# Kernel tuning notes

Measured on AMD Instinct MI355X. Metric: run time of the kernel, lower is better.

## Reference

```python
import jax, jax.numpy as jnp
import numpy as np


def setup_inputs() -> dict:
    key = jax.random.key(0)
    k1, k2 = jax.random.split(key)
    set1 = jax.random.normal(k1, (8192, 256), dtype=jnp.float32)
    set2 = jax.random.normal(k2, (8192, 256), dtype=jnp.float32)
    return {"set1": set1, "set2": set2}


def reference(set1, set2):
    # Pairwise Euclidean distances via the Gram trick:
    sq1 = jnp.sum(set1 * set1, axis=-1)  # [N]
    sq2 = jnp.sum(set2 * set2, axis=-1)  # [M]
    gram = jnp.einsum('nd,md->nm', set1, set2)  # [N,M]
    d2 = sq1[:, None] + sq2[None, :] - 2.0 * gram
    d = jnp.sqrt(jnp.maximum(d2, 0.0))  # clamp tiny negatives from roundoff
    term_1 = jnp.mean(jnp.min(d, axis=1))  # for each point in set1, nearest in set2
    term_2 = jnp.mean(jnp.min(d, axis=0))  # for each point in set2, nearest in set1
    return term_1 + term_2
```

## Files before the change

kernel.cpp:

```cpp
#include <hip/hip_runtime.h>

#define N_PTS 8192
#define D_DIM 256
#define BN 256
#define BM 128
#define BK 64
#define INF_BITS 0x7F800000u

typedef __attribute__((ext_vector_type(8))) short short8;
typedef __attribute__((ext_vector_type(4))) float f32x4;

__device__ __forceinline__ void gload_lds16(const ushort* g, ushort* l) {
    __builtin_amdgcn_global_load_lds(
        (const __attribute__((address_space(1))) void*)g,
        (__attribute__((address_space(3))) void*)l, 16, 0, 0);
}

__device__ __forceinline__ ushort f2bf(float x) {
    unsigned u = __float_as_uint(x);
    return (ushort)((u + 0x7FFFu + ((u >> 16) & 1u)) >> 16);
}

__global__ void prep_kernel(const float* __restrict__ s1, const float* __restrict__ s2,
                            ushort* __restrict__ b1, ushort* __restrict__ b2,
                            float* __restrict__ sq1, float* __restrict__ sq2,
                            unsigned* __restrict__ rowmin2, unsigned* __restrict__ colmin2) {
    const int half = N_PTS * D_DIM;
    int t = blockIdx.x * 256 + threadIdx.x;
    int e = t * 8;
    bool first = e < half;
    const float* src = first ? s1 : s2;
    ushort* dst = first ? b1 : b2;
    int off = first ? e : e - half;
    float4 v0 = *(const float4*)(src + off);
    float4 v1 = *(const float4*)(src + off + 4);
    float s = v0.x * v0.x + v0.y * v0.y + v0.z * v0.z + v0.w * v0.w
            + v1.x * v1.x + v1.y * v1.y + v1.z * v1.z + v1.w * v1.w;
    ushort4 o0 = { f2bf(v0.x), f2bf(v0.y), f2bf(v0.z), f2bf(v0.w) };
    ushort4 o1 = { f2bf(v1.x), f2bf(v1.y), f2bf(v1.z), f2bf(v1.w) };
    *(ushort4*)(dst + off)     = o0;
    *(ushort4*)(dst + off + 4) = o1;
    #pragma unroll
    for (int m = 1; m <= 16; m <<= 1) s += __shfl_xor(s, m, 64);
    int sub = threadIdx.x & 31;
    int row = off >> 8;
    if (sub == 0) (first ? sq1 : sq2)[row] = s;
    if (sub == 1) (first ? rowmin2 : colmin2)[row] = INF_BITS;
}

__global__ __launch_bounds__(256, 2) void tile_kernel(
    const ushort* __restrict__ B1, const ushort* __restrict__ B2,
    const float* __restrict__ sq1, const float* __restrict__ sq2,
    unsigned* __restrict__ rowmin2, unsigned* __restrict__ colmin2) {
    __shared__ ushort As[BN * BK] __attribute__((aligned(16)));
    __shared__ ushort Bs[BM * BK] __attribute__((aligned(16)));
    __shared__ unsigned rs[BN];
    __shared__ unsigned cs[BM];

    const int tid  = threadIdx.x;
    const int lane = tid & 63;
    const int w    = tid >> 6;
    const int quad = lane >> 4;
    const int c    = lane & 15;
    const int n_off = (w >> 1) * 128;
    const int m_off = (w & 1) * 64;
    const int n0 = blockIdx.y * BN;
    const int m0 = blockIdx.x * BM;

    rs[tid] = INF_BITS;
    if (tid < BM) cs[tid] = INF_BITS;

    f32x4 acc[8][4];
    #pragma unroll
    for (int ti = 0; ti < 8; ti++)
        #pragma unroll
        for (int tj = 0; tj < 4; tj++) acc[ti][tj] = (f32x4){0.f, 0.f, 0.f, 0.f};

    for (int k0 = 0; k0 < D_DIM; k0 += BK) {
        #pragma unroll
        for (int r = 0; r < 8; r++) {
            int idx = r * 256 + tid;
            int row = idx >> 3;
            int gc  = (idx & 7) ^ (row & 7);
            gload_lds16(B1 + (size_t)(n0 + row) * D_DIM + k0 + gc * 8,
                        &As[(idx & ~63) * 8]);
        }
        #pragma unroll
        for (int r = 0; r < 4; r++) {
            int idx = r * 256 + tid;
            int row = idx >> 3;
            int gc  = (idx & 7) ^ (row & 7);
            gload_lds16(B2 + (size_t)(m0 + row) * D_DIM + k0 + gc * 8,
                        &Bs[(idx & ~63) * 8]);
        }
        __syncthreads();

        #pragma unroll
        for (int kk = 0; kk < 2; kk++) {
            short8 a[8], b[4];
            #pragma unroll
            for (int ti = 0; ti < 8; ti++) {
                int row = n_off + ti * 16 + c;
                int ch  = (kk * 4 + quad) ^ (row & 7);
                a[ti] = *(const short8*)&As[row * BK + ch * 8];
            }
            #pragma unroll
            for (int tj = 0; tj < 4; tj++) {
                int row = m_off + tj * 16 + c;
                int ch  = (kk * 4 + quad) ^ (row & 7);
                b[tj] = *(const short8*)&Bs[row * BK + ch * 8];
            }
            #pragma unroll
            for (int ti = 0; ti < 8; ti++)
                #pragma unroll
                for (int tj = 0; tj < 4; tj++)
                    acc[ti][tj] = __builtin_amdgcn_mfma_f32_16x16x32_bf16(
                        a[ti], b[tj], acc[ti][tj], 0, 0, 0);
        }
        __syncthreads();
    }

    float sqm[4];
    #pragma unroll
    for (int tj = 0; tj < 4; tj++) sqm[tj] = sq2[m0 + m_off + tj * 16 + c];
    float cmin[4];
    #pragma unroll
    for (int tj = 0; tj < 4; tj++) cmin[tj] = __uint_as_float(INF_BITS);

    #pragma unroll
    for (int ti = 0; ti < 8; ti++) {
        float4 sqn = *(const float4*)&sq1[n0 + n_off + ti * 16 + quad * 4];
        float rmin[4] = { __uint_as_float(INF_BITS), __uint_as_float(INF_BITS),
                          __uint_as_float(INF_BITS), __uint_as_float(INF_BITS) };
        #pragma unroll
        for (int tj = 0; tj < 4; tj++) {
            float sn[4] = { sqn.x, sqn.y, sqn.z, sqn.w };
            #pragma unroll
            for (int r = 0; r < 4; r++) {
                float d2 = fmaxf(sn[r] + sqm[tj] - 2.f * acc[ti][tj][r], 0.f);
                rmin[r]  = fminf(rmin[r], d2);
                cmin[tj] = fminf(cmin[tj], d2);
            }
        }
        #pragma unroll
        for (int m = 1; m <= 8; m <<= 1)
            #pragma unroll
            for (int r = 0; r < 4; r++)
                rmin[r] = fminf(rmin[r], __shfl_xor(rmin[r], m, 64));
        if (c == 0) {
            #pragma unroll
            for (int r = 0; r < 4; r++)
                atomicMin(&rs[n_off + ti * 16 + quad * 4 + r], __float_as_uint(rmin[r]));
        }
    }
    #pragma unroll
    for (int m = 16; m <= 32; m <<= 1)
        #pragma unroll
        for (int tj = 0; tj < 4; tj++)
            cmin[tj] = fminf(cmin[tj], __shfl_xor(cmin[tj], m, 64));
    if (quad == 0) {
        #pragma unroll
        for (int tj = 0; tj < 4; tj++)
            atomicMin(&cs[m_off + tj * 16 + c], __float_as_uint(cmin[tj]));
    }
    __syncthreads();

    atomicMin(&rowmin2[n0 + tid], rs[tid]);
    if (tid < BM) atomicMin(&colmin2[m0 + tid], cs[tid]);
}

__global__ __launch_bounds__(1024) void reduce_kernel(const unsigned* __restrict__ mins,
                                                      float* __restrict__ out) {
    int tid = threadIdx.x;
    uint4 v[4];
    #pragma unroll
    for (int j = 0; j < 4; j++) v[j] = ((const uint4*)mins)[j * 1024 + tid];
    float s = 0.f;
    #pragma unroll
    for (int j = 0; j < 4; j++)
        s += sqrtf(__uint_as_float(v[j].x)) + sqrtf(__uint_as_float(v[j].y))
           + sqrtf(__uint_as_float(v[j].z)) + sqrtf(__uint_as_float(v[j].w));
    #pragma unroll
    for (int m = 32; m > 0; m >>= 1) s += __shfl_xor(s, m, 64);
    __shared__ float ws[16];
    int lane = tid & 63, wv = tid >> 6;
    if (lane == 0) ws[wv] = s;
    __syncthreads();
    if (tid < 16) {
        float t = ws[tid];
        #pragma unroll
        for (int m = 8; m > 0; m >>= 1) t += __shfl_xor(t, m, 64);
        if (tid == 0) out[0] = t / (float)N_PTS;
    }
}

extern "C" void kernel_launch(void* const* d_in, const int* in_sizes, int n_in,
                              void* d_out, int out_size, void* d_ws, size_t ws_size,
                              hipStream_t stream) {
    const float* set1 = (const float*)d_in[0];
    const float* set2 = (const float*)d_in[1];
    float* out = (float*)d_out;

    unsigned* rowmin2 = (unsigned*)d_ws;
    unsigned* colmin2 = rowmin2 + N_PTS;
    float* sq1 = (float*)(colmin2 + N_PTS);
    float* sq2 = sq1 + N_PTS;
    ushort* b1 = (ushort*)((char*)d_ws + 128 * 1024);
    ushort* b2 = b1 + (size_t)N_PTS * D_DIM;

    prep_kernel<<<(2 * N_PTS * D_DIM) / (256 * 8), 256, 0, stream>>>(
        set1, set2, b1, b2, sq1, sq2, rowmin2, colmin2);
    tile_kernel<<<dim3(N_PTS / BM, N_PTS / BN), 256, 0, stream>>>(
        b1, b2, sq1, sq2, rowmin2, colmin2);
    reduce_kernel<<<1, 1024, 0, stream>>>(rowmin2, out);
}
```

Baseline: 122.5 us.

## Keep set1 tile in registers and stream set2 directly from global without LDS

Replaces the LDS-staged 256x128 block GEMM with a register-resident scheme. Each wave holds its 64 set1 rows across the full 256-dim reduction in registers, then streams 64-row set2 chunks straight from global memory over 1024 columns. Row minima are accumulated across the whole sweep and column minima are sent to global atomics for each chunk. This drops shared-memory staging and barriers and shrinks the grid to 256 blocks, at the cost of heavy register pressure, uncoalesced per-lane global loads of set2 that rely on cache reuse, and more global atomics.

Result: slower. 167.0 us (+36.4%).

```diff
diff --git a/kernel.cpp b/kernel.cpp
--- a/kernel.cpp
+++ b/kernel.cpp
@@ -2,19 +2,10 @@
 
 #define N_PTS 8192
 #define D_DIM 256
-#define BN 256
-#define BM 128
-#define BK 64
 #define INF_BITS 0x7F800000u
 
 typedef __attribute__((ext_vector_type(8))) short short8;
 typedef __attribute__((ext_vector_type(4))) float f32x4;
-
-__device__ __forceinline__ void gload_lds16(const ushort* g, ushort* l) {
-    __builtin_amdgcn_global_load_lds(
-        (const __attribute__((address_space(1))) void*)g,
-        (__attribute__((address_space(3))) void*)l, 16, 0, 0);
-}
 
 __device__ __forceinline__ ushort f2bf(float x) {
     unsigned u = __float_as_uint(x);
@@ -52,121 +43,107 @@
     const ushort* __restrict__ B1, const ushort* __restrict__ B2,
     const float* __restrict__ sq1, const float* __restrict__ sq2,
     unsigned* __restrict__ rowmin2, unsigned* __restrict__ colmin2) {
-    __shared__ ushort As[BN * BK] __attribute__((aligned(16)));
-    __shared__ ushort Bs[BM * BK] __attribute__((aligned(16)));
-    __shared__ unsigned rs[BN];
-    __shared__ unsigned cs[BM];
+    const int tid   = threadIdx.x;
+    const int lane  = tid & 63;
+    const int w     = tid >> 6;
+    const int quad  = lane >> 4;
+    const int c     = lane & 15;
+    const int nbase = blockIdx.y * 256 + w * 64;
+    const int mbase = blockIdx.x * 1024;
 
-    const int tid  = threadIdx.x;
-    const int lane = tid & 63;
-    const int w    = tid >> 6;
-    const int quad = lane >> 4;
-    const int c    = lane & 15;
-    const int n_off = (w >> 1) * 128;
-    const int m_off = (w & 1) * 64;
-    const int n0 = blockIdx.y * BN;
-    const int m0 = blockIdx.x * BM;
+    short8 a[4][8];
+    #pragma unroll
+    for (int ti = 0; ti < 4; ti++)
+        #pragma unroll
+        for (int kc = 0; kc < 8; kc++)
+            a[ti][kc] = *(const short8*)(B1 + (size_t)(nbase + ti * 16 + c) * D_DIM
+                                         + kc * 32 + quad * 8);
 
-    rs[tid] = INF_BITS;
-    if (tid < BM) cs[tid] = INF_BITS;
+    float rmin[4][4];
+    #pragma unroll
+    for (int ti = 0; ti < 4; ti++)
+        #pragma unroll
+        for (int r = 0; r < 4; r++) rmin[ti][r] = __uint_as_float(INF_BITS);
 
-    f32x4 acc[8][4];
-    #pragma unroll
-    for (int ti = 0; ti < 8; ti++)
-        #pragma unroll
-        for (int tj = 0; tj < 4; tj++) acc[ti][tj] = (f32x4){0.f, 0.f, 0.f, 0.f};
+    const f32x4 z4 = {0.f, 0.f, 0.f, 0.f};
 
-    for (int k0 = 0; k0 < D_DIM; k0 += BK) {
-        #pragma unroll
-        for (int r = 0; r < 8; r++) {
-            int idx = r * 256 + tid;
-            int row = idx >> 3;
-            int gc  = (idx & 7) ^ (row & 7);
-            gload_lds16(B1 + (size_t)(n0 + row) * D_DIM + k0 + gc * 8,
-                        &As[(idx & ~63) * 8]);
-        }
-        #pragma unroll
-        for (int r = 0; r < 4; r++) {
-            int idx = r * 256 + tid;
-            int row = idx >> 3;
-            int gc  = (idx & 7) ^ (row & 7);
-            gload_lds16(B2 + (size_t)(m0 + row) * D_DIM + k0 + gc * 8,
-                        &Bs[(idx & ~63) * 8]);
-        }
-        __syncthreads();
-
-        #pragma unroll
-        for (int kk = 0; kk < 2; kk++) {
-            short8 a[8], b[4];
+    #pragma unroll 1
+    for (int mt = 0; mt < 16; mt++) {
+        const int m1 = mbase + mt * 64;
+        const ushort* bp = B2 + (size_t)m1 * D_DIM;
+        f32x4 acc[4][4];
+        {
+            short8 b[4];
             #pragma unroll
-            for (int ti = 0; ti < 8; ti++) {
-                int row = n_off + ti * 16 + c;
-                int ch  = (kk * 4 + quad) ^ (row & 7);
-                a[ti] = *(const short8*)&As[row * BK + ch * 8];
-            }
+            for (int tj = 0; tj < 4; tj++)
+                b[tj] = *(const short8*)(bp + (size_t)(tj * 16 + c) * D_DIM + quad * 8);
             #pragma unroll
-            for (int tj = 0; tj < 4; tj++) {
-                int row = m_off + tj * 16 + c;
-                int ch  = (kk * 4 + quad) ^ (row & 7);
-                b[tj] = *(const short8*)&Bs[row * BK + ch * 8];
-            }
-            #pragma unroll
-            for (int ti = 0; ti < 8; ti++)
+            for (int ti = 0; ti < 4; ti++)
                 #pragma unroll
                 for (int tj = 0; tj < 4; tj++)
                     acc[ti][tj] = __builtin_amdgcn_mfma_f32_16x16x32_bf16(
-                        a[ti], b[tj], acc[ti][tj], 0, 0, 0);
+                        a[ti][0], b[tj], z4, 0, 0, 0);
         }
-        __syncthreads();
+        #pragma unroll
+        for (int kc = 1; kc < 8; kc++) {
+            short8 b[4];
+            #pragma unroll
+            for (int tj = 0; tj < 4; tj++)
+                b[tj] = *(const short8*)(bp + (size_t)(tj * 16 + c) * D_DIM
+                                         + kc * 32 + quad * 8);
+            #pragma unroll
+            for (int ti = 0; ti < 4; ti++)
+                #pragma unroll
+                for (int tj = 0; tj < 4; tj++)
+                    acc[ti][tj] = __builtin_amdgcn_mfma_f32_16x16x32_bf16(
+                        a[ti][kc], b[tj], acc[ti][tj], 0, 0, 0);
+        }
+
+        float sqm[4];
+        #pragma unroll
+        for (int tj = 0; tj < 4; tj++) sqm[tj] = sq2[m1 + tj * 16 + c];
+        float cmin[4];
+        #pragma unroll
+        for (int tj = 0; tj < 4; tj++) cmin[tj] = __uint_as_float(INF_BITS);
+
+        #pragma unroll
+        for (int ti = 0; ti < 4; ti++) {
+            float4 sn = *(const float4*)&sq1[nbase + ti * 16 + quad * 4];
+            float snr[4] = { sn.x, sn.y, sn.z, sn.w };
+            #pragma unroll
+            for (int tj = 0; tj < 4; tj++)
+                #pragma unroll
+                for (int r = 0; r < 4; r++) {
+                    float d2 = fmaxf(snr[r] + sqm[tj] - 2.f * acc[ti][tj][r], 0.f);
+                    rmin[ti][r] = fminf(rmin[ti][r], d2);
+                    cmin[tj]    = fminf(cmin[tj], d2);
+                }
+        }
+        #pragma unroll
+        for (int m = 16; m <= 32; m <<= 1)
+            #pragma unroll
+            for (int tj = 0; tj < 4; tj++)
+                cmin[tj] = fminf(cmin[tj], __shfl_xor(cmin[tj], m, 64));
+        float cm = quad == 0 ? cmin[0] : quad == 1 ? cmin[1]
+                 : quad == 2 ? cmin[2] : cmin[3];
+        atomicMin(&colmin2[m1 + quad * 16 + c], __float_as_uint(cm));
     }
 
-    float sqm[4];
     #pragma unroll
-    for (int tj = 0; tj < 4; tj++) sqm[tj] = sq2[m0 + m_off + tj * 16 + c];
-    float cmin[4];
-    #pragma unroll
-    for (int tj = 0; tj < 4; tj++) cmin[tj] = __uint_as_float(INF_BITS);
-
-    #pragma unroll
-    for (int ti = 0; ti < 8; ti++) {
-        float4 sqn = *(const float4*)&sq1[n0 + n_off + ti * 16 + quad * 4];
-        float rmin[4] = { __uint_as_float(INF_BITS), __uint_as_float(INF_BITS),
-                          __uint_as_float(INF_BITS), __uint_as_float(INF_BITS) };
+    for (int m = 1; m <= 8; m <<= 1)
         #pragma unroll
-        for (int tj = 0; tj < 4; tj++) {
-            float sn[4] = { sqn.x, sqn.y, sqn.z, sqn.w };
-            #pragma unroll
-            for (int r = 0; r < 4; r++) {
-                float d2 = fmaxf(sn[r] + sqm[tj] - 2.f * acc[ti][tj][r], 0.f);
-                rmin[r]  = fminf(rmin[r], d2);
-                cmin[tj] = fminf(cmin[tj], d2);
-            }
-        }
-        #pragma unroll
-        for (int m = 1; m <= 8; m <<= 1)
+        for (int ti = 0; ti < 4; ti++)
             #pragma unroll
             for (int r = 0; r < 4; r++)
-                rmin[r] = fminf(rmin[r], __shfl_xor(rmin[r], m, 64));
-        if (c == 0) {
+                rmin[ti][r] = fminf(rmin[ti][r], __shfl_xor(rmin[ti][r], m, 64));
+    if (c == 0) {
+        #pragma unroll
+        for (int ti = 0; ti < 4; ti++)
             #pragma unroll
             for (int r = 0; r < 4; r++)
-                atomicMin(&rs[n_off + ti * 16 + quad * 4 + r], __float_as_uint(rmin[r]));
-        }
+                atomicMin(&rowmin2[nbase + ti * 16 + quad * 4 + r],
+                          __float_as_uint(rmin[ti][r]));
     }
-    #pragma unroll
-    for (int m = 16; m <= 32; m <<= 1)
-        #pragma unroll
-        for (int tj = 0; tj < 4; tj++)
-            cmin[tj] = fminf(cmin[tj], __shfl_xor(cmin[tj], m, 64));
-    if (quad == 0) {
-        #pragma unroll
-        for (int tj = 0; tj < 4; tj++)
-            atomicMin(&cs[m_off + tj * 16 + c], __float_as_uint(cmin[tj]));
-    }
-    __syncthreads();
-
-    atomicMin(&rowmin2[n0 + tid], rs[tid]);
-    if (tid < BM) atomicMin(&colmin2[m0 + tid], cs[tid]);
 }
 
 __global__ __launch_bounds__(1024) void reduce_kernel(const unsigned* __restrict__ mins,
@@ -210,7 +187,7 @@
 
     prep_kernel<<<(2 * N_PTS * D_DIM) / (256 * 8), 256, 0, stream>>>(
         set1, set2, b1, b2, sq1, sq2, rowmin2, colmin2);
-    tile_kernel<<<dim3(N_PTS / BM, N_PTS / BN), 256, 0, stream>>>(
+    tile_kernel<<<dim3(8, 32), 256, 0, stream>>>(
         b1, b2, sq1, sq2, rowmin2, colmin2);
     reduce_kernel<<<1, 1024, 0, stream>>>(rowmin2, out);
 }
```
